# Optimization experiments

Measured on AMD Instinct MI355X. Metric: run time of the kernel, lower is better.

The kernel has to match this reference:

```python
import jax, jax.numpy as jnp
import numpy as np

M, N, K, G = 8, 8192, 8192, 128  # tokens, out-features, in-features, quant group size
QMIN, QMAX = -8, 7               # 4-bit signed weight codes


def setup_inputs() -> dict:
    key = jax.random.key(0)
    k1, k2, k3, k4 = jax.random.split(key, 4)
    x = jax.random.normal(k1, (M, K), dtype=jnp.float32)
    # 4-bit signed weight codes stored as int32
    q_weight = jax.random.randint(k2, (N, K), QMIN, QMAX + 1, dtype=jnp.int32)
    # per-(row, group) scales, shape [N, K // G]
    scales = jax.random.uniform(k3, (N, K // G), dtype=jnp.float32,
                                minval=0.005, maxval=0.02)
    bias = jax.random.normal(k4, (N,), dtype=jnp.float32) * 0.1
    return {"x": x, "q_weight": q_weight, "scales": scales, "bias": bias}


def _fake_quant_act_int8(x):
    # dynamic per-token symmetric int8 quantization of activations
    s = jnp.max(jnp.abs(x), axis=-1, keepdims=True) / 127.0
    s = jnp.maximum(s, jnp.asarray(1e-8, x.dtype))
    q = jnp.clip(jnp.round(x / s), -127.0, 127.0)
    return q * s


def reference(x, q_weight, scales, bias):
    # x: [..., m, k] float; q_weight: [n, k] int 4-bit codes; scales: [n, k/G]
    xq = _fake_quant_act_int8(x)
    n, k = q_weight.shape
    g = k // scales.shape[1]
    # per-group dequantize weight: [n, k/g, g] * [n, k/g, 1] -> [n, k]
    w = (q_weight.reshape(n, -1, g).astype(x.dtype) * scales[:, :, None]).reshape(n, k)
    out = jnp.einsum('mk,nk->mn', xq, w)  # [m, n]
    return out + bias
```

## Files before the change

kernel.cpp:

```cpp
#include <hip/hip_runtime.h>
#include <math.h>

constexpr int M_TOK = 8;
constexpr int N_OUT = 8192;
constexpr int K_IN  = 8192;
constexpr int KG    = 64;
constexpr int R_N   = 4;

typedef int   i32x4 __attribute__((ext_vector_type(4)));
typedef float f32x4 __attribute__((ext_vector_type(4)));

__global__ __launch_bounds__(1024) void act_quant_kernel(const float* __restrict__ x,
                                                         float* __restrict__ xq) {
    const int row = blockIdx.x;
    const f32x4* xr = reinterpret_cast<const f32x4*>(x + (size_t)row * K_IN);
    f32x4* oq = reinterpret_cast<f32x4*>(xq + (size_t)row * K_IN);
    const int tid = threadIdx.x;

    f32x4 v0 = xr[tid * 2];
    f32x4 v1 = xr[tid * 2 + 1];

    float m = fmaxf(
        fmaxf(fmaxf(fabsf(v0.x), fabsf(v0.y)), fmaxf(fabsf(v0.z), fabsf(v0.w))),
        fmaxf(fmaxf(fabsf(v1.x), fabsf(v1.y)), fmaxf(fabsf(v1.z), fabsf(v1.w))));

    #pragma unroll
    for (int off = 32; off; off >>= 1) m = fmaxf(m, __shfl_xor(m, off));

    __shared__ float smax[16];
    if ((tid & 63) == 0) smax[tid >> 6] = m;
    __syncthreads();
    float mm = smax[0];
    #pragma unroll
    for (int i = 1; i < 16; ++i) mm = fmaxf(mm, smax[i]);

    const float s = fmaxf(mm / 127.0f, 1e-8f);

    auto quant = [&](float v) -> float {
        float q = rintf(v / s);
        q = fminf(fmaxf(q, -127.0f), 127.0f);
        return q * s;
    };

    f32x4 o0, o1;
    o0.x = quant(v0.x); o0.y = quant(v0.y); o0.z = quant(v0.z); o0.w = quant(v0.w);
    o1.x = quant(v1.x); o1.y = quant(v1.y); o1.z = quant(v1.z); o1.w = quant(v1.w);
    oq[tid * 2]     = o0;
    oq[tid * 2 + 1] = o1;
}

__global__ __launch_bounds__(256) void qlin_kernel(const float* __restrict__ xq,
                                                   const int* __restrict__ qw,
                                                   const float* __restrict__ scales,
                                                   const float* __restrict__ bias,
                                                   float* __restrict__ out) {
    const int wave = blockIdx.x * 4 + (threadIdx.x >> 6);
    const int lane = threadIdx.x & 63;
    const int n0 = wave * R_N;
    const int lk = lane * 4;
    const int phase = (wave & 255) * 32;

    float acc[R_N][M_TOK];
    #pragma unroll
    for (int r = 0; r < R_N; ++r)
        #pragma unroll
        for (int m = 0; m < M_TOK; ++m) acc[r][m] = 0.0f;

    for (int t = 0; t < 32; ++t) {
        const int k = (phase + t * 256 + lk) & (K_IN - 1);
        const int g = k >> 7;

        f32x4 xv[M_TOK];
        #pragma unroll
        for (int m = 0; m < M_TOK; ++m)
            xv[m] = *reinterpret_cast<const f32x4*>(xq + (size_t)m * K_IN + k);

        #pragma unroll
        for (int r = 0; r < R_N; ++r) {
            const i32x4 c =
                *reinterpret_cast<const i32x4*>(qw + (size_t)(n0 + r) * K_IN + k);
            const float sc = scales[(size_t)(n0 + r) * KG + g];
            const float w0 = (float)c.x * sc;
            const float w1 = (float)c.y * sc;
            const float w2 = (float)c.z * sc;
            const float w3 = (float)c.w * sc;
            #pragma unroll
            for (int m = 0; m < M_TOK; ++m) {
                float a = acc[r][m];
                a = fmaf(w0, xv[m].x, a);
                a = fmaf(w1, xv[m].y, a);
                a = fmaf(w2, xv[m].z, a);
                a = fmaf(w3, xv[m].w, a);
                acc[r][m] = a;
            }
        }
    }

    #pragma unroll
    for (int r = 0; r < R_N; ++r)
        #pragma unroll
        for (int m = 0; m < M_TOK; ++m) {
            float v = acc[r][m];
            #pragma unroll
            for (int off = 32; off; off >>= 1) v += __shfl_xor(v, off);
            acc[r][m] = v;
        }

    if (lane < R_N * M_TOK) {
        const int rsel = lane >> 3;
        const int msel = lane & 7;
        float myv = 0.0f;
        #pragma unroll
        for (int r = 0; r < R_N; ++r)
            #pragma unroll
            for (int m = 0; m < M_TOK; ++m)
                if (r == rsel && m == msel) myv = acc[r][m];
        out[(size_t)msel * N_OUT + n0 + rsel] = myv + bias[n0 + rsel];
    }
}

extern "C" void kernel_launch(void* const* d_in, const int* in_sizes, int n_in,
                              void* d_out, int out_size, void* d_ws, size_t ws_size,
                              hipStream_t stream) {
    const float* x      = (const float*)d_in[0];
    const int*   qw     = (const int*)d_in[1];
    const float* scales = (const float*)d_in[2];
    const float* bias   = (const float*)d_in[3];
    float* out = (float*)d_out;
    float* xq  = (float*)d_ws;

    act_quant_kernel<<<M_TOK, 1024, 0, stream>>>(x, xq);

    const int waves  = N_OUT / R_N;
    const int blocks = waves / 4;
    qlin_kernel<<<blocks, 256, 0, stream>>>(xq, qw, scales, bias, out);
}
```

Before: 56.82 us.

## Store activations as int8 codes and stage them in LDS per block

The activation quantizer now emits packed int8 codes plus a per-row scale instead of dequantized floats. The linear kernel copies all int8 activations into shared memory at block start, unpacks them to floats in the inner loop, and applies the row scale in the epilogue. This cuts activation read bytes, but it adds a 64 KB shared-memory stage per block that limits occupancy and adds unpack work on a weight-bandwidth-bound loop.

```diff
diff --git a/kernel.cpp b/kernel.cpp
--- a/kernel.cpp
+++ b/kernel.cpp
@@ -11,10 +11,10 @@
 typedef float f32x4 __attribute__((ext_vector_type(4)));
 
 __global__ __launch_bounds__(1024) void act_quant_kernel(const float* __restrict__ x,
-                                                         float* __restrict__ xq) {
+                                                         signed char* __restrict__ xq8,
+                                                         float* __restrict__ srow) {
     const int row = blockIdx.x;
     const f32x4* xr = reinterpret_cast<const f32x4*>(x + (size_t)row * K_IN);
-    f32x4* oq = reinterpret_cast<f32x4*>(xq + (size_t)row * K_IN);
     const int tid = threadIdx.x;
 
     f32x4 v0 = xr[tid * 2];
@@ -35,30 +35,47 @@
     for (int i = 1; i < 16; ++i) mm = fmaxf(mm, smax[i]);
 
     const float s = fmaxf(mm / 127.0f, 1e-8f);
+    if (tid == 0) srow[row] = s;
 
-    auto quant = [&](float v) -> float {
+    auto qcode = [&](float v) -> int {
         float q = rintf(v / s);
         q = fminf(fmaxf(q, -127.0f), 127.0f);
-        return q * s;
+        return (int)q;
     };
 
-    f32x4 o0, o1;
-    o0.x = quant(v0.x); o0.y = quant(v0.y); o0.z = quant(v0.z); o0.w = quant(v0.w);
-    o1.x = quant(v1.x); o1.y = quant(v1.y); o1.z = quant(v1.z); o1.w = quant(v1.w);
-    oq[tid * 2]     = o0;
-    oq[tid * 2 + 1] = o1;
+    const int q0 = qcode(v0.x) & 255, q1 = qcode(v0.y) & 255,
+              q2 = qcode(v0.z) & 255, q3 = qcode(v0.w) & 255;
+    const int q4 = qcode(v1.x) & 255, q5 = qcode(v1.y) & 255,
+              q6 = qcode(v1.z) & 255, q7 = qcode(v1.w) & 255;
+    int2 p;
+    p.x = q0 | (q1 << 8) | (q2 << 16) | (q3 << 24);
+    p.y = q4 | (q5 << 8) | (q6 << 16) | (q7 << 24);
+    reinterpret_cast<int2*>(xq8 + (size_t)row * K_IN)[tid] = p;
 }
 
-__global__ __launch_bounds__(256) void qlin_kernel(const float* __restrict__ xq,
+__global__ __launch_bounds__(256) void qlin_kernel(const signed char* __restrict__ xq8,
+                                                   const float* __restrict__ srow,
                                                    const int* __restrict__ qw,
                                                    const float* __restrict__ scales,
                                                    const float* __restrict__ bias,
                                                    float* __restrict__ out) {
-    const int wave = blockIdx.x * 4 + (threadIdx.x >> 6);
+    __shared__ int xsm[M_TOK * K_IN / 4];
+
+    const int widx = threadIdx.x >> 6;
     const int lane = threadIdx.x & 63;
+    const int wave = blockIdx.x * 4 + widx;
     const int n0 = wave * R_N;
     const int lk = lane * 4;
     const int phase = (wave & 255) * 32;
+
+    {
+        const i32x4* src = reinterpret_cast<const i32x4*>(xq8);
+        i32x4* dst = reinterpret_cast<i32x4*>(xsm);
+        #pragma unroll
+        for (int j = 0; j < 16; ++j)
+            dst[j * 256 + threadIdx.x] = src[j * 256 + threadIdx.x];
+    }
+    __syncthreads();
 
     float acc[R_N][M_TOK];
     #pragma unroll
@@ -69,11 +86,17 @@
     for (int t = 0; t < 32; ++t) {
         const int k = (phase + t * 256 + lk) & (K_IN - 1);
         const int g = k >> 7;
+        const int kd = k >> 2;
 
         f32x4 xv[M_TOK];
         #pragma unroll
-        for (int m = 0; m < M_TOK; ++m)
-            xv[m] = *reinterpret_cast<const f32x4*>(xq + (size_t)m * K_IN + k);
+        for (int m = 0; m < M_TOK; ++m) {
+            const int d = xsm[m * 2048 + kd];
+            xv[m].x = (float)((d << 24) >> 24);
+            xv[m].y = (float)((d << 16) >> 24);
+            xv[m].z = (float)((d << 8) >> 24);
+            xv[m].w = (float)(d >> 24);
+        }
 
         #pragma unroll
         for (int r = 0; r < R_N; ++r) {
@@ -114,7 +137,7 @@
         for (int r = 0; r < R_N; ++r)
             #pragma unroll
             for (int m = 0; m < M_TOK; ++m)
-                if (r == rsel && m == msel) myv = acc[r][m];
+                if (r == rsel && m == msel) myv = acc[r][m] * srow[m];
         out[(size_t)msel * N_OUT + n0 + rsel] = myv + bias[n0 + rsel];
     }
 }
@@ -127,11 +150,13 @@
     const float* scales = (const float*)d_in[2];
     const float* bias   = (const float*)d_in[3];
     float* out = (float*)d_out;
-    float* xq  = (float*)d_ws;
 
-    act_quant_kernel<<<M_TOK, 1024, 0, stream>>>(x, xq);
+    float*       srow = (float*)d_ws;
+    signed char* xq8  = (signed char*)d_ws + 256;
+
+    act_quant_kernel<<<M_TOK, 1024, 0, stream>>>(x, xq8, srow);
 
     const int waves  = N_OUT / R_N;
     const int blocks = waves / 4;
-    qlin_kernel<<<blocks, 256, 0, stream>>>(xq, qw, scales, bias, out);
+    qlin_kernel<<<blocks, 256, 0, stream>>>(xq8, srow, qw, scales, bias, out);
 }
```

Measured after the change: 55.19 us. -2.9%, faster.
